# Kernel optimization log

Hardware: AMD Instinct MI355X
Metric: run time of the kernel (lower is better)

The kernel has to match this reference:

```python
import jax, jax.numpy as jnp
import numpy as np

B, N, C = 8, 4096, 768
NUM_HEADS = 8
HEAD_DIM = C // NUM_HEADS
FOCUSING_FACTOR = 3


def setup_inputs() -> dict:
    key = jax.random.key(0)
    ks = jax.random.split(key, 8)
    x = jax.random.normal(ks[0], (B, N, C), dtype=jnp.float32)
    Wq = jax.random.normal(ks[1], (C, C), dtype=jnp.float32) * 0.02
    Wkv = jax.random.normal(ks[2], (C, C), dtype=jnp.float32) * 0.02
    Wproj = jax.random.normal(ks[3], (C, C), dtype=jnp.float32) * 0.02
    bproj = jnp.zeros((C,), dtype=jnp.float32)
    w_g = jax.random.normal(ks[4], (C, 1), dtype=jnp.float32)
    # scale / positional_encoding are zero-init Parameters; use small random
    # values so the numerics are non-trivial for kernel testing.
    scale_p = jax.random.normal(ks[5], (1, 1, C), dtype=jnp.float32) * 0.02
    pos_enc = jax.random.normal(ks[6], (1, N, C), dtype=jnp.float32) * 0.02
    return {"x": x, "H": 64, "W": 64, "Wq": Wq, "Wkv": Wkv,
            "Wproj": Wproj, "bproj": bproj, "w_g": w_g,
            "scale_p": scale_p, "pos_enc": pos_enc}


def _l2norm(v, axis):
    return jnp.sqrt(jnp.sum(v * v, axis=axis, keepdims=True))


def reference(x, H, W, Wq, Wkv, Wproj, bproj, w_g, scale_p, pos_enc):
    Bx, Nx, Cx = x.shape
    scale_factor = HEAD_DIM ** (-0.5)
    q = jnp.einsum('bnc,dc->bnd', x, Wq)      # (B,N,C)
    k = jnp.einsum('bnc,dc->bnd', x, Wkv)     # kv -> k
    # global aggregation weight
    A = (q @ w_g) * scale_factor              # (B,N,1)
    A = A / jnp.maximum(_l2norm(A, axis=1), 1e-12)  # F.normalize over dim=1
    G = jnp.sum(A * q, axis=1)                # (B,C)
    xg = G[:, None, :] * k                    # (B,N,C)
    k = k + pos_enc
    # focusing feature map
    scale = jax.nn.softplus(scale_p)
    q = (jax.nn.relu(q) + 1e-6) / scale
    k = (jax.nn.relu(k) + 1e-6) / scale
    q_norm = _l2norm(q, axis=-1)
    k_norm = _l2norm(k, axis=-1)
    q = q ** FOCUSING_FACTOR
    k = k ** FOCUSING_FACTOR
    q = q / _l2norm(q, axis=-1) * q_norm
    k = k / _l2norm(k, axis=-1) * k_norm
    # split heads: (B, H, N, d)
    q = q.reshape(Bx, Nx, NUM_HEADS, HEAD_DIM).transpose(0, 2, 1, 3)
    k = k.reshape(Bx, Nx, NUM_HEADS, HEAD_DIM).transpose(0, 2, 1, 3)
    k_mean = k.mean(axis=2)                   # (B,H,d)
    z = 1.0 / (jnp.einsum('bhnd,bhd->bhn', q, k_mean)[..., None] + 1e-6)
    xg = xg.reshape(Bx, Nx, NUM_HEADS, HEAD_DIM).transpose(0, 2, 1, 3)
    xg = xg * z                               # (B,H,N,d)
    out = xg.transpose(0, 2, 1, 3).reshape(Bx, Nx, Cx)
    out = jnp.einsum('bnc,dc->bnd', out, Wproj) + bproj
    return out
```

## Files before the change

kernel.cpp:

```cpp
#include <hip/hip_runtime.h>
#include <hip/hip_bf16.h>
#include <cstdint>
#include <cstddef>


#define GLOAD_LDS16(g, l) \
  __builtin_amdgcn_global_load_lds((const __attribute__((address_space(1))) void*)(g), \
                                   (__attribute__((address_space(3))) void*)(l), 16, 0, 0)

typedef __attribute__((ext_vector_type(8))) short bf16x8;
typedef __attribute__((ext_vector_type(4))) float f32x4;

__device__ __forceinline__ ushort f2bf(float f) {
  union { float f; uint32_t u; } v; v.f = f;
  uint32_t r = v.u + 0x7fffu + ((v.u >> 16) & 1u);
  return (ushort)(r >> 16);
}
__device__ __forceinline__ float bf2f(ushort u) {
  union { uint32_t x; float f; } v; v.x = (uint32_t)u << 16; return v.f;
}

__global__ __launch_bounds__(256) void k_conv(const float* __restrict__ src,
                                              ushort* __restrict__ dst, int n4) {
  int i = blockIdx.x * blockDim.x + threadIdx.x;
  int stride = gridDim.x * blockDim.x;
  for (; i < n4; i += stride) {
    float4 v = ((const float4*)src)[i];
    ushort4 o;
    o.x = f2bf(v.x); o.y = f2bf(v.y); o.z = f2bf(v.z); o.w = f2bf(v.w);
    ((ushort4*)dst)[i] = o;
  }
}

__global__ void k_softplus(const float* __restrict__ p, float* __restrict__ sinv) {
  int i = threadIdx.x + blockIdx.x * 256;
  if (i < 768) {
    float x = p[i];
    float s = (x > 20.f) ? x : log1pf(expf(x));
    sinv[i] = 1.0f / s;
  }
}

template <bool BF16OUT>
__global__ __launch_bounds__(256, 2) void gemm_bt(
    const ushort* __restrict__ A, const ushort* __restrict__ Bt,
    void* __restrict__ Cv, const float* __restrict__ bias, int Ncols) {
  constexpr int K = 768, BK = 64;
  __shared__ ushort lA[128 * BK];
  __shared__ ushort lB[128 * BK];
  const int tid  = threadIdx.x;
  const int lane = tid & 63;
  const int w    = tid >> 6;
  const int wr   = w >> 1, wc = w & 1;
  const int m0 = blockIdx.y * 128;
  const int n0 = blockIdx.x * 128;
  const int sr = lane >> 3;
  const int sc = (lane & 7) * 8;

  f32x4 acc[4][4] = {};

  for (int kt = 0; kt < K / BK; ++kt) {
    const int k0 = kt * BK;
    __syncthreads();
#pragma unroll
    for (int i = 0; i < 4; ++i) {
      const int ci = w * 4 + i;
      const int r  = ci * 8 + sr;
      GLOAD_LDS16(A  + (size_t)(m0 + r) * K + (k0 + sc), lA + ci * 512);
      GLOAD_LDS16(Bt + (size_t)(n0 + r) * K + (k0 + sc), lB + ci * 512);
    }
    __syncthreads();
#pragma unroll
    for (int kk = 0; kk < BK / 32; ++kk) {
      bf16x8 af[4], bfr[4];
#pragma unroll
      for (int m = 0; m < 4; ++m)
        af[m] = *(const bf16x8*)&lA[(wr * 64 + m * 16 + (lane & 15)) * BK + kk * 32 + (lane >> 4) * 8];
#pragma unroll
      for (int n = 0; n < 4; ++n)
        bfr[n] = *(const bf16x8*)&lB[(wc * 64 + n * 16 + (lane & 15)) * BK + kk * 32 + (lane >> 4) * 8];
#pragma unroll
      for (int m = 0; m < 4; ++m)
#pragma unroll
        for (int n = 0; n < 4; ++n)
          acc[m][n] = __builtin_amdgcn_mfma_f32_16x16x32_bf16(af[m], bfr[n], acc[m][n], 0, 0, 0);
    }
  }
#pragma unroll
  for (int n = 0; n < 4; ++n) {
    const int col = n0 + wc * 64 + n * 16 + (lane & 15);
    const float bv = (!BF16OUT && bias) ? bias[col] : 0.0f;
#pragma unroll
    for (int m = 0; m < 4; ++m) {
      const int row0 = m0 + wr * 64 + m * 16 + (lane >> 4) * 4;
#pragma unroll
      for (int j = 0; j < 4; ++j) {
        if (BF16OUT)
          ((ushort*)Cv)[(size_t)(row0 + j) * Ncols + col] = f2bf(acc[m][n][j]);
        else
          ((float*)Cv)[(size_t)(row0 + j) * Ncols + col] = acc[m][n][j] + bv;
      }
    }
  }
}

__global__ __launch_bounds__(256) void k_gks(const ushort* __restrict__ qk,
                                             const float* __restrict__ pos,
                                             const float* __restrict__ wg,
                                             const float* __restrict__ sinv,
                                             float* __restrict__ part,
                                             float* __restrict__ partW) {
  __shared__ float pG[4][768];
  __shared__ float pK[4][768];
  __shared__ float lsq[4];
  const int tid = threadIdx.x, lane = tid & 63, w = tid >> 6;
  const int c0 = lane * 12;
  float sv[12], wv[12], ga[12] = {}, ka[12] = {};
#pragma unroll
  for (int v = 0; v < 3; ++v) {
    float4 s = *(const float4*)(sinv + c0 + v * 4);
    float4 g = *(const float4*)(wg + c0 + v * 4);
#pragma unroll
    for (int e = 0; e < 4; ++e) { sv[v * 4 + e] = (&s.x)[e]; wv[v * 4 + e] = (&g.x)[e]; }
  }
  float wsq = 0.f;
  for (int r = 0; r < 8; ++r) {
    const int row = blockIdx.x * 32 + w * 8 + r;
    const ushort* qr = qk + (size_t)row * 1536;
    const float* pr = pos + (size_t)(row & 4095) * 768;
    float q[12], kk[12], u[12];
    float d = 0.f, s1 = 0.f, s2 = 0.f;
#pragma unroll
    for (int v = 0; v < 3; ++v) {
      ushort4 qv = *(const ushort4*)(qr + c0 + v * 4);
      ushort4 kv = *(const ushort4*)(qr + 768 + c0 + v * 4);
      float4 pv = *(const float4*)(pr + c0 + v * 4);
#pragma unroll
      for (int e = 0; e < 4; ++e) {
        const int j = v * 4 + e;
        q[j] = bf2f((&qv.x)[e]);
        kk[j] = bf2f((&kv.x)[e]) + (&pv.x)[e];
      }
    }
#pragma unroll
    for (int j = 0; j < 12; ++j) {
      d += q[j] * wv[j];
      float t = (fmaxf(kk[j], 0.f) + 1e-6f) * sv[j];
      float uu = t * t * t;
      u[j] = uu;
      s1 += t * t; s2 += uu * uu;
    }
#pragma unroll
    for (int m = 32; m; m >>= 1) {
      d += __shfl_xor(d, m); s1 += __shfl_xor(s1, m); s2 += __shfl_xor(s2, m);
    }
    const float ratio = sqrtf(s1 / s2);
    wsq += d * d;
#pragma unroll
    for (int j = 0; j < 12; ++j) { ka[j] += u[j] * ratio; ga[j] += d * q[j]; }
  }
#pragma unroll
  for (int j = 0; j < 12; ++j) { pG[w][c0 + j] = ga[j]; pK[w][c0 + j] = ka[j]; }
  if (lane == 0) lsq[w] = wsq;
  __syncthreads();
  float* outp = part + (size_t)blockIdx.x * 1536;
  for (int i = tid; i < 768; i += 256) {
    outp[i]       = pG[0][i] + pG[1][i] + pG[2][i] + pG[3][i];
    outp[768 + i] = pK[0][i] + pK[1][i] + pK[2][i] + pK[3][i];
  }
  if (tid == 0) partW[blockIdx.x] = lsq[0] + lsq[1] + lsq[2] + lsq[3];
}

__global__ __launch_bounds__(256) void k_rnorm(const float* __restrict__ partW,
                                               float* __restrict__ rnorm) {
  const int tid = threadIdx.x;
  const int b = tid >> 5, j = tid & 31;
  float s = 0.f;
#pragma unroll
  for (int v = 0; v < 4; ++v) s += partW[b * 128 + j * 4 + v];
#pragma unroll
  for (int m = 16; m; m >>= 1) s += __shfl_xor(s, m);
  if (j == 0) {
    const float sf = 0.10206207261596575f;
    rnorm[b] = sf / fmaxf(sf * sqrtf(s), 1e-12f);
  }
}

__global__ __launch_bounds__(256) void k_gred(const float* __restrict__ part,
                                              const float* __restrict__ rnorm,
                                              float* __restrict__ G,
                                              float* __restrict__ ksum) {
  const int i = blockIdx.x * 256 + threadIdx.x;
  const int b = blockIdx.y;
  const float* p = part + (size_t)b * 128 * 1536 + i;
  float s = 0.f;
#pragma unroll 8
  for (int blk = 0; blk < 128; ++blk) s += p[(size_t)blk * 1536];
  if (i < 768) G[b * 768 + i] = s * rnorm[b];
  else         ksum[b * 768 + i - 768] = s;
}

__global__ __launch_bounds__(256) void k_y(const ushort* __restrict__ qk,
                                           const float* __restrict__ G,
                                           const float* __restrict__ ksum,
                                           const float* __restrict__ sinv,
                                           ushort* __restrict__ y) {
  const int tid = threadIdx.x, lane = tid & 63, w = tid >> 6;
  const int row = blockIdx.x * 4 + w;
  const int b = row >> 12;
  const int c0 = lane * 12;
  const ushort* qr = qk + (size_t)row * 1536;
  float kk[12], u[12], ks[12], gg[12];
  float s1 = 0.f, s2 = 0.f;
#pragma unroll
  for (int v = 0; v < 3; ++v) {
    ushort4 qv = *(const ushort4*)(qr + c0 + v * 4);
    ushort4 kv = *(const ushort4*)(qr + 768 + c0 + v * 4);
    float4 sv = *(const float4*)(sinv + c0 + v * 4);
    float4 kv2 = *(const float4*)(ksum + b * 768 + c0 + v * 4);
    float4 gv = *(const float4*)(G + b * 768 + c0 + v * 4);
#pragma unroll
    for (int e = 0; e < 4; ++e) {
      const int j = v * 4 + e;
      kk[j] = bf2f((&kv.x)[e]);
      float t = (fmaxf(bf2f((&qv.x)[e]), 0.f) + 1e-6f) * (&sv.x)[e];
      float uu = t * t * t;
      u[j] = uu; s1 += t * t; s2 += uu * uu;
      ks[j] = (&kv2.x)[e]; gg[j] = (&gv.x)[e];
    }
  }
#pragma unroll
  for (int m = 32; m; m >>= 1) { s1 += __shfl_xor(s1, m); s2 += __shfl_xor(s2, m); }
  const float ratio = sqrtf(s1 / s2);
  float zp = 0.f;
#pragma unroll
  for (int j = 0; j < 12; ++j) zp += u[j] * ks[j];
  zp += __shfl_xor(zp, 1); zp += __shfl_xor(zp, 2); zp += __shfl_xor(zp, 4);
  const float z = 1.0f / (ratio * zp * (1.0f / 4096.0f) + 1e-6f);
  ushort o[12];
#pragma unroll
  for (int j = 0; j < 12; ++j) o[j] = f2bf(gg[j] * kk[j] * z);
  ushort* yp = y + (size_t)row * 768 + c0;
#pragma unroll
  for (int v = 0; v < 3; ++v)
    *(ushort4*)(yp + v * 4) = *(ushort4*)(o + v * 4);
}

extern "C" void kernel_launch(void* const* d_in, const int* in_sizes, int n_in,
                              void* d_out, int out_size, void* d_ws, size_t ws_size,
                              hipStream_t stream) {
  const float* x      = (const float*)d_in[0];
  const float* Wq     = (const float*)d_in[3];
  const float* Wkv    = (const float*)d_in[4];
  const float* Wproj  = (const float*)d_in[5];
  const float* bproj  = (const float*)d_in[6];
  const float* wg     = (const float*)d_in[7];
  const float* scalep = (const float*)d_in[8];
  const float* pos    = (const float*)d_in[9];

  char* ws = (char*)d_ws;
  ushort* qk   = (ushort*)ws;
  ushort* xbf  = (ushort*)(ws + 100663296);
  ushort* ybf  = xbf;
  float*  part = (float*)(ws + 100663296);
  ushort* wqk  = (ushort*)(ws + 150994944);
  ushort* wpj  = (ushort*)(ws + 153354240);
  float*  sinv = (float*)(ws + 154533888);
  float*  partW = (float*)(ws + 154536960);
  float*  accb  = (float*)(ws + 154541056);
  float* Gv     = accb;
  float* ksum   = accb + 6144;
  float* rnorm  = accb + 12288;

  k_conv<<<4096, 256, 0, stream>>>(x, xbf, 25165824 / 4);
  k_conv<<<576, 256, 0, stream>>>(Wq, wqk, 589824 / 4);
  k_conv<<<576, 256, 0, stream>>>(Wkv, wqk + 589824, 589824 / 4);
  k_conv<<<576, 256, 0, stream>>>(Wproj, wpj, 589824 / 4);
  k_softplus<<<3, 256, 0, stream>>>(scalep, sinv);

  gemm_bt<true><<<dim3(12, 256), 256, 0, stream>>>(xbf, wqk, qk, nullptr, 1536);

  k_gks<<<1024, 256, 0, stream>>>(qk, pos, wg, sinv, part, partW);
  k_rnorm<<<1, 256, 0, stream>>>(partW, rnorm);
  k_gred<<<dim3(6, 8), 256, 0, stream>>>(part, rnorm, Gv, ksum);
  k_y<<<8192, 256, 0, stream>>>(qk, Gv, ksum, sinv, ybf);

  gemm_bt<false><<<dim3(6, 256), 256, 0, stream>>>(ybf, wpj, d_out, bproj, 768);
}
```

Measured before the change: 423.6 us.

## Fuse x bf16 conversion into QK GEMM loads and swizzle block mapping

Removes the standalone fp32-to-bf16 conversion pass over the input activations by converting inside the QK GEMM's A-tile load, writing bf16 to LDS directly. Both GEMMs switch to a 1D grid with a swizzled block-to-tile mapping that groups blocks by blockIdx modulo 8 to improve cache locality across dies. The trade-off is that the A loads go through registers rather than async global-to-LDS transfers, and fp32 x is read repeatedly per column block.

```diff
diff --git a/kernel.cpp b/kernel.cpp
--- a/kernel.cpp
+++ b/kernel.cpp
@@ -41,10 +41,10 @@
   }
 }
 
-template <bool BF16OUT>
+template <bool BF16OUT, bool CONVA>
 __global__ __launch_bounds__(256, 2) void gemm_bt(
-    const ushort* __restrict__ A, const ushort* __restrict__ Bt,
-    void* __restrict__ Cv, const float* __restrict__ bias, int Ncols) {
+    const void* __restrict__ Av, const ushort* __restrict__ Bt,
+    void* __restrict__ Cv, const float* __restrict__ bias, int Ncols, int nbx) {
   constexpr int K = 768, BK = 64;
   __shared__ ushort lA[128 * BK];
   __shared__ ushort lB[128 * BK];
@@ -52,8 +52,10 @@
   const int lane = tid & 63;
   const int w    = tid >> 6;
   const int wr   = w >> 1, wc = w & 1;
-  const int m0 = blockIdx.y * 128;
-  const int n0 = blockIdx.x * 128;
+  const int cpx  = gridDim.x >> 3;
+  const int swz  = (blockIdx.x & 7) * cpx + (blockIdx.x >> 3);
+  const int m0 = (swz / nbx) * 128;
+  const int n0 = (swz % nbx) * 128;
   const int sr = lane >> 3;
   const int sc = (lane & 7) * 8;
 
@@ -66,7 +68,18 @@
     for (int i = 0; i < 4; ++i) {
       const int ci = w * 4 + i;
       const int r  = ci * 8 + sr;
-      GLOAD_LDS16(A  + (size_t)(m0 + r) * K + (k0 + sc), lA + ci * 512);
+      if constexpr (CONVA) {
+        const float* src = (const float*)Av + (size_t)(m0 + r) * K + (k0 + sc);
+        float4 v0 = *(const float4*)src;
+        float4 v1 = *(const float4*)(src + 4);
+        ushort4 o0, o1;
+        o0.x = f2bf(v0.x); o0.y = f2bf(v0.y); o0.z = f2bf(v0.z); o0.w = f2bf(v0.w);
+        o1.x = f2bf(v1.x); o1.y = f2bf(v1.y); o1.z = f2bf(v1.z); o1.w = f2bf(v1.w);
+        *(ushort4*)&lA[ci * 512 + lane * 8]     = o0;
+        *(ushort4*)&lA[ci * 512 + lane * 8 + 4] = o1;
+      } else {
+        GLOAD_LDS16((const ushort*)Av + (size_t)(m0 + r) * K + (k0 + sc), lA + ci * 512);
+      }
       GLOAD_LDS16(Bt + (size_t)(n0 + r) * K + (k0 + sc), lB + ci * 512);
     }
     __syncthreads();
@@ -260,9 +273,8 @@
 
   char* ws = (char*)d_ws;
   ushort* qk   = (ushort*)ws;
-  ushort* xbf  = (ushort*)(ws + 100663296);
-  ushort* ybf  = xbf;
   float*  part = (float*)(ws + 100663296);
+  ushort* ybf  = (ushort*)(ws + 100663296);
   ushort* wqk  = (ushort*)(ws + 150994944);
   ushort* wpj  = (ushort*)(ws + 153354240);
   float*  sinv = (float*)(ws + 154533888);
@@ -272,18 +284,17 @@
   float* ksum   = accb + 6144;
   float* rnorm  = accb + 12288;
 
-  k_conv<<<4096, 256, 0, stream>>>(x, xbf, 25165824 / 4);
   k_conv<<<576, 256, 0, stream>>>(Wq, wqk, 589824 / 4);
   k_conv<<<576, 256, 0, stream>>>(Wkv, wqk + 589824, 589824 / 4);
   k_conv<<<576, 256, 0, stream>>>(Wproj, wpj, 589824 / 4);
   k_softplus<<<3, 256, 0, stream>>>(scalep, sinv);
 
-  gemm_bt<true><<<dim3(12, 256), 256, 0, stream>>>(xbf, wqk, qk, nullptr, 1536);
+  gemm_bt<true, true><<<3072, 256, 0, stream>>>(x, wqk, qk, nullptr, 1536, 12);
 
   k_gks<<<1024, 256, 0, stream>>>(qk, pos, wg, sinv, part, partW);
   k_rnorm<<<1, 256, 0, stream>>>(partW, rnorm);
   k_gred<<<dim3(6, 8), 256, 0, stream>>>(part, rnorm, Gv, ksum);
   k_y<<<8192, 256, 0, stream>>>(qk, Gv, ksum, sinv, ybf);
 
-  gemm_bt<false><<<dim3(6, 256), 256, 0, stream>>>(ybf, wpj, d_out, bproj, 768);
-}
+  gemm_bt<false, false><<<1536, 256, 0, stream>>>(ybf, wpj, d_out, bproj, 768, 6);
+}
```

After: 467.9 us. 1.1x slower.
